# Kernel tuning notes

Hardware: AMD Instinct MI355X
Metric: run time of the kernel (lower is better)

Reference implementation:

```python
import jax, jax.numpy as jnp
import numpy as np

BITS = 4
GROUP_SIZE = 128
IN_FEATURES = 4096
OUT_FEATURES = 4096
ELEMS_PER_BYTE = 8 // BITS  # 2


def make_lut():
    # lut1 = linspace(-1, 1, 2^bits); lut = cartesian product over packed elems -> [256, 2]
    lut1 = np.linspace(-1.0, 1.0, 2 ** BITS, dtype=np.float32)
    hi, lo = np.meshgrid(lut1, lut1, indexing='ij')  # first elem is high nibble
    return jnp.asarray(np.stack([hi.ravel(), lo.ravel()], axis=-1))  # [256, 2]


def setup_inputs() -> dict:
    key = jax.random.key(0)
    k1, k2, k3 = jax.random.split(key, 3)
    x = jax.random.normal(k1, (8, 2048, IN_FEATURES), dtype=jnp.float32)
    # packed 4-bit weights: one byte holds 2 indices
    weight_data = jax.random.randint(k2, (OUT_FEATURES, IN_FEATURES // ELEMS_PER_BYTE), 0, 256, dtype=jnp.int32)
    # per-group scales (amax for 4-bit), strictly positive
    scale = jax.random.uniform(k3, (OUT_FEATURES, IN_FEATURES // GROUP_SIZE), dtype=jnp.float32, minval=0.01, maxval=1.0)
    lut = make_lut()
    return {"x": x, "weight_data": weight_data, "scale": scale, "lut": lut}


def reference(x, weight_data, scale, lut):
    O, n_bytes = weight_data.shape
    n_groups = scale.shape[1]
    # LUT gather: each packed byte -> ELEMS_PER_BYTE dequantised values in [-1, 1]
    w = lut[weight_data]                      # [O, I/2, 2]
    w = w.reshape(O, n_groups, -1)            # [O, I/g, g]
    w = w * scale[:, :, None]                 # per-group rescale
    w = w.reshape(O, -1)                      # [O, I]
    # y = x @ W^T over flattened leading dims
    return jnp.einsum('...i,oi->...o', x, w)
```

## Files before the change

kernel.cpp:

```cpp
#include <hip/hip_runtime.h>
#include <hip/hip_bf16.h>

#define M_DIM 16384
#define N_DIM 4096
#define K_DIM 4096

typedef __attribute__((ext_vector_type(8))) short short8_t;
typedef __attribute__((ext_vector_type(4))) float float4_t;
typedef __attribute__((ext_vector_type(4))) int int4_t;

__device__ __forceinline__ short f2bf(float f) {
    union { __hip_bfloat16 b; short s; } u;
    u.b = __float2bfloat16(f);
    return u.s;
}

__global__ __launch_bounds__(256) void conv_x(const float* __restrict__ x,
                                              short* __restrict__ xb) {
    size_t t = (size_t)blockIdx.x * 256 + threadIdx.x;
    const float4_t a = __builtin_nontemporal_load((const float4_t*)(x + t * 8));
    const float4_t b = __builtin_nontemporal_load((const float4_t*)(x + t * 8 + 4));
    short8_t v;
    v[0] = f2bf(a[0]); v[1] = f2bf(a[1]); v[2] = f2bf(a[2]); v[3] = f2bf(a[3]);
    v[4] = f2bf(b[0]); v[5] = f2bf(b[1]); v[6] = f2bf(b[2]); v[7] = f2bf(b[3]);
    *(short8_t*)(xb + t * 8) = v;
}

__global__ __launch_bounds__(256) void dequant_w(const int* __restrict__ wd,
                                                 const float* __restrict__ scale,
                                                 const float* __restrict__ lut,
                                                 short* __restrict__ Wq) {
    int t = blockIdx.x * 256 + threadIdx.x;
    int row = t >> 9;
    int cb  = t & 511;
    const int4_t w4 = __builtin_nontemporal_load(
        (const int4_t*)&wd[(size_t)row * 2048 + cb * 4]);
    const float s = scale[row * 32 + (cb >> 4)];
    int idx[4] = {w4[0], w4[1], w4[2], w4[3]};
    short8_t v;
#pragma unroll
    for (int j = 0; j < 4; ++j) {
        v[2 * j + 0] = f2bf(lut[idx[j] * 2 + 0] * s);
        v[2 * j + 1] = f2bf(lut[idx[j] * 2 + 1] * s);
    }
    *(short8_t*)&Wq[(size_t)row * K_DIM + cb * 8] = v;
}

#define LOADA(MH, BUF) \
  _Pragma("unroll") for (int q = 0; q < 4; ++q) { \
    afr[q][0] = *(const short8_t*)(smem + ABASE + (BUF) + ((MH)*4+q)*1024); \
    afr[q][1] = *(const short8_t*)(smem + ABASE + (BUF) + 8192 + ((MH)*4+q)*1024); }

#define LOADB(NH, BUF) \
  _Pragma("unroll") for (int q = 0; q < 2; ++q) { \
    bfr[q][0] = *(const short8_t*)(smem + BBASE + (BUF) + ((NH)*2+q)*1024); \
    bfr[q][1] = *(const short8_t*)(smem + BBASE + (BUF) + 8192 + ((NH)*2+q)*1024); }

#define MFMAQ(MH, NH) \
  _Pragma("unroll") for (int q = 0; q < 4; ++q) \
  _Pragma("unroll") for (int p = 0; p < 2; ++p) { \
    acc[(MH)*4+q][(NH)*2+p] = __builtin_amdgcn_mfma_f32_16x16x32_bf16(afr[q][0], bfr[p][0], acc[(MH)*4+q][(NH)*2+p], 0, 0, 0); \
    acc[(MH)*4+q][(NH)*2+p] = __builtin_amdgcn_mfma_f32_16x16x32_bf16(afr[q][1], bfr[p][1], acc[(MH)*4+q][(NH)*2+p], 0, 0, 0); }

#define STAGE_F(P, GOFF, DOFF) \
  __builtin_amdgcn_global_load_lds((const __attribute__((address_space(1))) void*)((P) + (GOFF)), \
      (__attribute__((address_space(3))) void*)(smem + (DOFF) + f0), 16, 0, 0); \
  __builtin_amdgcn_global_load_lds((const __attribute__((address_space(1))) void*)((P) + (GOFF) + 64), \
      (__attribute__((address_space(3))) void*)(smem + (DOFF) + 8192 + f0), 16, 0, 0);

#define VM4 asm volatile("s_waitcnt vmcnt(4)" ::: "memory");
#define VM0 asm volatile("s_waitcnt vmcnt(0)" ::: "memory");

#define PH2(LOADS, MH, NH, STG, WAITV) \
    LOADS \
    STG \
    __builtin_amdgcn_s_barrier(); \
    asm volatile("s_waitcnt lgkmcnt(0)" ::: "memory"); \
    __builtin_amdgcn_s_setprio(1); \
    MFMAQ(MH, NH); \
    __builtin_amdgcn_s_setprio(0); \
    WAITV \
    __builtin_amdgcn_s_barrier();


__global__ __launch_bounds__(512, 2) void gemm8(const short* __restrict__ A,
                                                const short* __restrict__ B,
                                                float* __restrict__ C) {
    __shared__ __align__(16) char smem[131072];
    const int tid = threadIdx.x;
    const int lane = tid & 63;
    const int wid = tid >> 6;
    const int wr = wid >> 2, wc = wid & 3;
    const int lr = lane & 15;
    const int lk2 = ((lane >> 4) << 3) * 2;
    const int swz5 = ((lr >> 3) & 1) << 5;

    const int xcd = blockIdx.x & 7;
    const int p   = blockIdx.x >> 3;
    const int bm  = xcd * 8 + (p & 7);
    const int bn  = p >> 3;

    const int ABASE = wr * 16384 + lr * 64 + (lk2 ^ swz5);
    const int BBASE = 65536 + (wc >> 1) * 16384 + (wc & 1) * 4096 + lr * 64 + (lk2 ^ swz5);

    const int f0 = tid * 16;
    const int rr0 = tid >> 2;
    const int cs0 = (f0 & 63) ^ (((f0 >> 9) & 1) << 5);

    const char* pA0 = (const char*)A + ((size_t)(bm * 256 + rr0) * K_DIM) * 2 + cs0;
    const char* pA1 = pA0 + (size_t)128 * K_DIM * 2;
    const char* pB0 = (const char*)B + ((size_t)(bn * 256 + rr0) * K_DIM) * 2 + cs0;
    const char* pB1 = pB0 + (size_t)128 * K_DIM * 2;

    float4_t acc[8][4] = {};
    short8_t afr[4][2], bfr[2][2];

    STAGE_F(pA0, 0,   0)
    STAGE_F(pB1, 0,   81920)
    STAGE_F(pA1, 0,   16384)
    STAGE_F(pB0, 0,   65536)
    STAGE_F(pA0, 128, 32768)
    STAGE_F(pB1, 128, 114688)
    STAGE_F(pA1, 128, 49152)
    STAGE_F(pB0, 128, 98304)
    asm volatile("s_waitcnt vmcnt(8)" ::: "memory");
    __builtin_amdgcn_s_barrier();

    PH2(LOADA(0,0) LOADB(0,0), 0, 0, , )
    PH2(LOADB(1,0),            0, 1, , )
    PH2(LOADA(1,0),            1, 1, STAGE_F(pA0, 256, 0),      )
    PH2(LOADB(0,0),            1, 0, STAGE_F(pB1, 256, 81920),  VM4)
    PH2(LOADA(0,32768) LOADB(0,32768), 0, 0, STAGE_F(pA1, 256, 16384), )
    PH2(LOADB(1,32768),                0, 1, STAGE_F(pB0, 256, 65536), )
    PH2(LOADA(1,32768),                1, 1, STAGE_F(pA0, 384, 32768), )
    PH2(LOADB(0,32768),                1, 0, STAGE_F(pB1, 384, 114688), VM4)
    pA0 += 256; pA1 += 256; pB0 += 256; pB1 += 256;

#pragma unroll 1
    for (int t = 1; t < 31; ++t) {
        PH2(LOADA(0,0) LOADB(0,0), 0, 0, STAGE_F(pA1, 128, 49152),  )
        PH2(LOADB(1,0),            0, 1, STAGE_F(pB0, 128, 98304),  )
        PH2(LOADA(1,0),            1, 1, STAGE_F(pA0, 256, 0),      )
        PH2(LOADB(0,0),            1, 0, STAGE_F(pB1, 256, 81920),  VM4)
        PH2(LOADA(0,32768) LOADB(0,32768), 0, 0, STAGE_F(pA1, 256, 16384), )
        PH2(LOADB(1,32768),                0, 1, STAGE_F(pB0, 256, 65536), )
        PH2(LOADA(1,32768),                1, 1, STAGE_F(pA0, 384, 32768), )
        PH2(LOADB(0,32768),                1, 0, STAGE_F(pB1, 384, 114688), VM4)
        pA0 += 256; pA1 += 256; pB0 += 256; pB1 += 256;
    }

    PH2(LOADA(0,0) LOADB(0,0), 0, 0, STAGE_F(pA1, 128, 49152), )
    PH2(LOADB(1,0),            0, 1, STAGE_F(pB0, 128, 98304), )
    PH2(LOADA(1,0),            1, 1, , )
    PH2(LOADB(0,0),            1, 0, , VM0)
    PH2(LOADA(0,32768) LOADB(0,32768), 0, 0, , )
    PH2(LOADB(1,32768),                0, 1, , )
    PH2(LOADA(1,32768),                1, 1, , )
    PH2(LOADB(0,32768),                1, 0, , )

    const int orow0 = bm * 256 + wr * 128;
    const int ocol0 = bn * 256 + wc * 64 + lr;
    const int rsub = (lane >> 4) << 2;
#pragma unroll
    for (int mi = 0; mi < 8; ++mi) {
#pragma unroll
        for (int r = 0; r < 4; ++r) {
            int row = orow0 + mi * 16 + rsub + r;
            float* cp = C + (size_t)row * N_DIM + ocol0;
#pragma unroll
            for (int ni = 0; ni < 4; ++ni)
                __builtin_nontemporal_store(acc[mi][ni][r], cp + ni * 16);
        }
    }
}

__global__ __launch_bounds__(256) void gemm_fb(const float* __restrict__ A,
                                               const short* __restrict__ B,
                                               float* __restrict__ C) {
    __shared__ short Al[128 * 32];
    __shared__ short Bl[128 * 32];
    const int bid0 = blockIdx.x;
    const int bid = (bid0 & 7) * 512 + (bid0 >> 3);
    const int bm = bid >> 5, bn = bid & 31;
    const int tid = threadIdx.x;
    const int lane = tid & 63;
    const int w = tid >> 6;
    const int wr = w >> 1, wc = w & 1;
    const int lr = lane & 15;
    const int lk = (lane >> 4) << 3;
    float4_t acc[4][4] = {};
    for (int k0 = 0; k0 < K_DIM; k0 += 32) {
        __syncthreads();
#pragma unroll
        for (int i = 0; i < 2; ++i) {
            int e = i * 2048 + tid * 8;
            int row = e >> 5, col = e & 31;
            const float* gp = A + (size_t)(bm * 128 + row) * K_DIM + k0 + col;
            float4 fa = *(const float4*)gp;
            float4 fb = *(const float4*)(gp + 4);
            short8_t v;
            v[0] = f2bf(fa.x); v[1] = f2bf(fa.y); v[2] = f2bf(fa.z); v[3] = f2bf(fa.w);
            v[4] = f2bf(fb.x); v[5] = f2bf(fb.y); v[6] = f2bf(fb.z); v[7] = f2bf(fb.w);
            *(short8_t*)&Al[e] = v;
        }
#pragma unroll
        for (int i = 0; i < 2; ++i) {
            int f = i * 4096 + tid * 16;
            int row = f >> 6, colb = f & 63;
            const char* gb = (const char*)B + ((size_t)(bn * 128 + row) * K_DIM + k0) * 2 + colb;
            __builtin_amdgcn_global_load_lds(
                (const __attribute__((address_space(1))) void*)gb,
                (__attribute__((address_space(3))) void*)((char*)Bl + f), 16, 0, 0);
        }
        __syncthreads();
        short8_t af[4], bf[4];
#pragma unroll
        for (int mi = 0; mi < 4; ++mi)
            af[mi] = *(const short8_t*)&Al[(wr * 64 + mi * 16 + lr) * 32 + lk];
#pragma unroll
        for (int ni = 0; ni < 4; ++ni)
            bf[ni] = *(const short8_t*)&Bl[(wc * 64 + ni * 16 + lr) * 32 + lk];
#pragma unroll
        for (int mi = 0; mi < 4; ++mi)
#pragma unroll
            for (int ni = 0; ni < 4; ++ni)
                acc[mi][ni] = __builtin_amdgcn_mfma_f32_16x16x32_bf16(af[mi], bf[ni], acc[mi][ni], 0, 0, 0);
    }
    const int orow0 = bm * 128 + wr * 64;
    const int ocol0 = bn * 128 + wc * 64 + (lane & 15);
#pragma unroll
    for (int mi = 0; mi < 4; ++mi)
#pragma unroll
        for (int r = 0; r < 4; ++r) {
            int row = orow0 + mi * 16 + ((lane >> 4) << 2) + r;
            float* cp = C + (size_t)row * N_DIM + ocol0;
#pragma unroll
            for (int ni = 0; ni < 4; ++ni)
                cp[ni * 16] = acc[mi][ni][r];
        }
}

extern "C" void kernel_launch(void* const* d_in, const int* in_sizes, int n_in,
                              void* d_out, int out_size, void* d_ws, size_t ws_size,
                              hipStream_t stream) {
    const float* x     = (const float*)d_in[0];
    const int*   wd    = (const int*)d_in[1];
    const float* scale = (const float*)d_in[2];
    const float* lut   = (const float*)d_in[3];
    float* out = (float*)d_out;

    const size_t wq_bytes = (size_t)N_DIM * K_DIM * 2;
    const size_t xb_bytes = (size_t)M_DIM * K_DIM * 2;
    short* Wq = (short*)d_ws;
    short* xb = (short*)((char*)d_ws + wq_bytes);
    const bool have_xb = ws_size >= wq_bytes + xb_bytes;

    if (have_xb) {
        conv_x<<<32768, 256, 0, stream>>>(x, xb);
        dequant_w<<<8192, 256, 0, stream>>>(wd, scale, lut, Wq);
        gemm8<<<(M_DIM / 256) * (N_DIM / 256), 512, 0, stream>>>(xb, Wq, out);
    } else {
        dequant_w<<<8192, 256, 0, stream>>>(wd, scale, lut, Wq);
        gemm_fb<<<(M_DIM / 128) * (N_DIM / 128), 256, 0, stream>>>(x, Wq, out);
    }
}
```

Measured before the change: 556.6 us.

## Double-buffer LDS fragment registers to overlap ds_reads with MFMA phases

Splits the A/B register fragments into two sets so the next phase's LDS reads are issued while the current phase's MFMAs run. Partial lgkmcnt waits and sched_barriers enforce the ordering. The epilogue stores also switch from nontemporal to plain stores. This aims to hide LDS read latency behind matrix math, at the cost of more VGPRs, which could cause spills or lower occupancy at launch_bounds(512,2).

Measured after the change: 563.1 us. No clear change (+1.2%).

```diff
diff --git a/kernel.cpp b/kernel.cpp
--- a/kernel.cpp
+++ b/kernel.cpp
@@ -46,21 +46,27 @@
     *(short8_t*)&Wq[(size_t)row * K_DIM + cb * 8] = v;
 }
 
-#define LOADA(MH, BUF) \
+#define LOADA_TO(DST, MH, BUF) \
   _Pragma("unroll") for (int q = 0; q < 4; ++q) { \
-    afr[q][0] = *(const short8_t*)(smem + ABASE + (BUF) + ((MH)*4+q)*1024); \
-    afr[q][1] = *(const short8_t*)(smem + ABASE + (BUF) + 8192 + ((MH)*4+q)*1024); }
-
-#define LOADB(NH, BUF) \
+    DST[q][0] = *(const short8_t*)(smem + ABASE + (BUF) + ((MH)*4+q)*1024); \
+    DST[q][1] = *(const short8_t*)(smem + ABASE + (BUF) + 8192 + ((MH)*4+q)*1024); }
+
+#define LOADB_TO(DST, NH, BUF) \
   _Pragma("unroll") for (int q = 0; q < 2; ++q) { \
-    bfr[q][0] = *(const short8_t*)(smem + BBASE + (BUF) + ((NH)*2+q)*1024); \
-    bfr[q][1] = *(const short8_t*)(smem + BBASE + (BUF) + 8192 + ((NH)*2+q)*1024); }
-
-#define MFMAQ(MH, NH) \
+    DST[q][0] = *(const short8_t*)(smem + BBASE + (BUF) + ((NH)*2+q)*1024); \
+    DST[q][1] = *(const short8_t*)(smem + BBASE + (BUF) + 8192 + ((NH)*2+q)*1024); }
+
+#define PRE1(BUF) \
+  LOADA_TO(afr0, 0, BUF) \
+  LOADB_TO(bfr0, 0, BUF) \
+  __builtin_amdgcn_sched_barrier(0); \
+  LOADB_TO(bfr1, 1, BUF)
+
+#define MFMAQ(MH, NH, AF, BF) \
   _Pragma("unroll") for (int q = 0; q < 4; ++q) \
   _Pragma("unroll") for (int p = 0; p < 2; ++p) { \
-    acc[(MH)*4+q][(NH)*2+p] = __builtin_amdgcn_mfma_f32_16x16x32_bf16(afr[q][0], bfr[p][0], acc[(MH)*4+q][(NH)*2+p], 0, 0, 0); \
-    acc[(MH)*4+q][(NH)*2+p] = __builtin_amdgcn_mfma_f32_16x16x32_bf16(afr[q][1], bfr[p][1], acc[(MH)*4+q][(NH)*2+p], 0, 0, 0); }
+    acc[(MH)*4+q][(NH)*2+p] = __builtin_amdgcn_mfma_f32_16x16x32_bf16(AF[q][0], BF[p][0], acc[(MH)*4+q][(NH)*2+p], 0, 0, 0); \
+    acc[(MH)*4+q][(NH)*2+p] = __builtin_amdgcn_mfma_f32_16x16x32_bf16(AF[q][1], BF[p][1], acc[(MH)*4+q][(NH)*2+p], 0, 0, 0); }
 
 #define STAGE_F(P, GOFF, DOFF) \
   __builtin_amdgcn_global_load_lds((const __attribute__((address_space(1))) void*)((P) + (GOFF)), \
@@ -71,13 +77,14 @@
 #define VM4 asm volatile("s_waitcnt vmcnt(4)" ::: "memory");
 #define VM0 asm volatile("s_waitcnt vmcnt(0)" ::: "memory");
 
-#define PH2(LOADS, MH, NH, STG, WAITV) \
-    LOADS \
+#define PHY(PRE, STG, LG, MH, NH, AF, BF, WAITV) \
+    PRE \
     STG \
     __builtin_amdgcn_s_barrier(); \
-    asm volatile("s_waitcnt lgkmcnt(0)" ::: "memory"); \
+    asm volatile("s_waitcnt lgkmcnt(" LG ")" ::: "memory"); \
+    __builtin_amdgcn_sched_barrier(0); \
     __builtin_amdgcn_s_setprio(1); \
-    MFMAQ(MH, NH); \
+    MFMAQ(MH, NH, AF, BF); \
     __builtin_amdgcn_s_setprio(0); \
     WAITV \
     __builtin_amdgcn_s_barrier();
@@ -113,7 +120,8 @@
     const char* pB1 = pB0 + (size_t)128 * K_DIM * 2;
 
     float4_t acc[8][4] = {};
-    short8_t afr[4][2], bfr[2][2];
+    short8_t afr0[4][2], afr1[4][2];
+    short8_t bfr0[2][2], bfr1[2][2];
 
     STAGE_F(pA0, 0,   0)
     STAGE_F(pB1, 0,   81920)
@@ -126,37 +134,37 @@
     asm volatile("s_waitcnt vmcnt(8)" ::: "memory");
     __builtin_amdgcn_s_barrier();
 
-    PH2(LOADA(0,0) LOADB(0,0), 0, 0, , )
-    PH2(LOADB(1,0),            0, 1, , )
-    PH2(LOADA(1,0),            1, 1, STAGE_F(pA0, 256, 0),      )
-    PH2(LOADB(0,0),            1, 0, STAGE_F(pB1, 256, 81920),  VM4)
-    PH2(LOADA(0,32768) LOADB(0,32768), 0, 0, STAGE_F(pA1, 256, 16384), )
-    PH2(LOADB(1,32768),                0, 1, STAGE_F(pB0, 256, 65536), )
-    PH2(LOADA(1,32768),                1, 1, STAGE_F(pA0, 384, 32768), )
-    PH2(LOADB(0,32768),                1, 0, STAGE_F(pB1, 384, 114688), VM4)
+    PHY(PRE1(0),                 ,                       "4", 0,0, afr0,bfr0, )
+    PHY(LOADA_TO(afr1,1,0),      ,                       "8", 0,1, afr0,bfr1, )
+    PHY(LOADB_TO(bfr0,0,0),      STAGE_F(pA0,256,0),     "4", 1,1, afr1,bfr1, )
+    PHY(,                        STAGE_F(pB1,256,81920), "0", 1,0, afr1,bfr0, VM4)
+    PHY(PRE1(32768),             STAGE_F(pA1,256,16384), "4", 0,0, afr0,bfr0, )
+    PHY(LOADA_TO(afr1,1,32768),  STAGE_F(pB0,256,65536), "8", 0,1, afr0,bfr1, )
+    PHY(LOADB_TO(bfr0,0,32768),  STAGE_F(pA0,384,32768), "4", 1,1, afr1,bfr1, )
+    PHY(,                        STAGE_F(pB1,384,114688),"0", 1,0, afr1,bfr0, VM4)
     pA0 += 256; pA1 += 256; pB0 += 256; pB1 += 256;
 
 #pragma unroll 1
     for (int t = 1; t < 31; ++t) {
-        PH2(LOADA(0,0) LOADB(0,0), 0, 0, STAGE_F(pA1, 128, 49152),  )
-        PH2(LOADB(1,0),            0, 1, STAGE_F(pB0, 128, 98304),  )
-        PH2(LOADA(1,0),            1, 1, STAGE_F(pA0, 256, 0),      )
-        PH2(LOADB(0,0),            1, 0, STAGE_F(pB1, 256, 81920),  VM4)
-        PH2(LOADA(0,32768) LOADB(0,32768), 0, 0, STAGE_F(pA1, 256, 16384), )
-        PH2(LOADB(1,32768),                0, 1, STAGE_F(pB0, 256, 65536), )
-        PH2(LOADA(1,32768),                1, 1, STAGE_F(pA0, 384, 32768), )
-        PH2(LOADB(0,32768),                1, 0, STAGE_F(pB1, 384, 114688), VM4)
+        PHY(PRE1(0),                 STAGE_F(pA1,128,49152),  "4", 0,0, afr0,bfr0, )
+        PHY(LOADA_TO(afr1,1,0),      STAGE_F(pB0,128,98304),  "8", 0,1, afr0,bfr1, )
+        PHY(LOADB_TO(bfr0,0,0),      STAGE_F(pA0,256,0),      "4", 1,1, afr1,bfr1, )
+        PHY(,                        STAGE_F(pB1,256,81920),  "0", 1,0, afr1,bfr0, VM4)
+        PHY(PRE1(32768),             STAGE_F(pA1,256,16384),  "4", 0,0, afr0,bfr0, )
+        PHY(LOADA_TO(afr1,1,32768),  STAGE_F(pB0,256,65536),  "8", 0,1, afr0,bfr1, )
+        PHY(LOADB_TO(bfr0,0,32768),  STAGE_F(pA0,384,32768),  "4", 1,1, afr1,bfr1, )
+        PHY(,                        STAGE_F(pB1,384,114688), "0", 1,0, afr1,bfr0, VM4)
         pA0 += 256; pA1 += 256; pB0 += 256; pB1 += 256;
     }
 
-    PH2(LOADA(0,0) LOADB(0,0), 0, 0, STAGE_F(pA1, 128, 49152), )
-    PH2(LOADB(1,0),            0, 1, STAGE_F(pB0, 128, 98304), )
-    PH2(LOADA(1,0),            1, 1, , )
-    PH2(LOADB(0,0),            1, 0, , VM0)
-    PH2(LOADA(0,32768) LOADB(0,32768), 0, 0, , )
-    PH2(LOADB(1,32768),                0, 1, , )
-    PH2(LOADA(1,32768),                1, 1, , )
-    PH2(LOADB(0,32768),                1, 0, , )
+    PHY(PRE1(0),                 STAGE_F(pA1,128,49152), "4", 0,0, afr0,bfr0, )
+    PHY(LOADA_TO(afr1,1,0),      STAGE_F(pB0,128,98304), "8", 0,1, afr0,bfr1, )
+    PHY(LOADB_TO(bfr0,0,0),      ,                       "4", 1,1, afr1,bfr1, )
+    PHY(,                        ,                       "0", 1,0, afr1,bfr0, VM0)
+    PHY(PRE1(32768),             , "4", 0,0, afr0,bfr0, )
+    PHY(LOADA_TO(afr1,1,32768),  , "8", 0,1, afr0,bfr1, )
+    PHY(LOADB_TO(bfr0,0,32768),  , "4", 1,1, afr1,bfr1, )
+    PHY(,                        , "0", 1,0, afr1,bfr0, )
 
     const int orow0 = bm * 256 + wr * 128;
     const int ocol0 = bn * 256 + wc * 64 + lr;
@@ -169,7 +177,7 @@
             float* cp = C + (size_t)row * N_DIM + ocol0;
 #pragma unroll
             for (int ni = 0; ni < 4; ++ni)
-                __builtin_nontemporal_store(acc[mi][ni][r], cp + ni * 16);
+                cp[ni * 16] = acc[mi][ni][r];
         }
     }
 }
```
